# Kernel optimization log

Measured on AMD Instinct MI355X. Metric: run time of the kernel, lower is better.

## Reference

```python
import jax, jax.numpy as jnp
import numpy as np

B, T, D_MODEL, D_FF, NUM_EXPERTS, TOP_K = 8, 4096, 512, 2048, 8, 2
VOCAB = 50257


def setup_inputs() -> dict:
    key = jax.random.key(0)
    k_x, k_id, k_w1, k_w2 = jax.random.split(key, 4)
    x = jax.random.normal(k_x, (B, T, D_MODEL), dtype=jnp.float32)
    token_ids = jax.random.randint(k_id, (B, T), 0, VOCAB, dtype=jnp.int32)
    # stacked expert MLP params: Linear(D,F) -> GELU -> Linear(F,D)
    W1 = jax.random.normal(k_w1, (NUM_EXPERTS, D_MODEL, D_FF), dtype=jnp.float32) * 0.02
    b1 = jnp.zeros((NUM_EXPERTS, D_FF), dtype=jnp.float32)
    W2 = jax.random.normal(k_w2, (NUM_EXPERTS, D_FF, D_MODEL), dtype=jnp.float32) * 0.02
    b2 = jnp.zeros((NUM_EXPERTS, D_MODEL), dtype=jnp.float32)
    return {"x": x, "token_ids": token_ids, "W1": W1, "b1": b1, "W2": W2, "b2": b2}


def reference(x, token_ids, W1, b1, W2, b2):
    Bx, Tx, D = x.shape
    E = W1.shape[0]
    top_k = TOP_K
    # hash routing: expert_ids[b,t,k] = (b*T + token_ids[b,t] + k) % E
    rows = (jnp.arange(Bx, dtype=jnp.int32) * Tx)[:, None, None]           # (B,1,1)
    offs = jnp.arange(top_k, dtype=jnp.int32)                               # (K,)
    expert_ids = (rows + token_ids[:, :, None] + offs) % E                  # (B,T,K)
    onehot = jax.nn.one_hot(expert_ids, E, dtype=jnp.float32)               # (B,T,K,E)
    hits = onehot.sum(axis=2)                                               # (B,T,E) hit counts
    # per-hit combine weight in torch source: (1/top_k)/top_k = 1/top_k^2
    comb_w = hits / float(top_k * top_k)
    # masked-dense expert MLP == dense MLP on x with output masked (per-token ops)
    out = jnp.zeros_like(x)
    for e in range(E):  # fixed small loop over experts
        h = jax.nn.gelu(x @ W1[e] + b1[e], approximate=False)               # (B,T,F)
        y = h @ W2[e] + b2[e]                                               # (B,T,D)
        out = out + y * comb_w[..., e:e + 1]
    expert_counts = hits.sum(axis=(0, 1))                                   # (E,)
    return out, expert_ids, expert_counts
```

## Files before the change

kernel.cpp:

```cpp
#include <hip/hip_runtime.h>
#include <math.h>

#define NUM_E 8
#define NTOK  32768
#define TSEQ  4096
#define DM    512
#define DF    2048
#define CAP   6144

typedef unsigned short ushort_t;
typedef __attribute__((ext_vector_type(8))) short short8;
typedef __attribute__((ext_vector_type(4))) float floatx4;

__device__ __forceinline__ unsigned short f2bf(float f){
  union { float f; unsigned int u; } v; v.f = f;
  unsigned int u = v.u;
  unsigned int r = (u + 0x7FFFu + ((u >> 16) & 1u)) >> 16;
  return (unsigned short)r;
}

__device__ __forceinline__ float gelu_fast(float h){
  float z = h * (1.5957691216057308f + 0.0713548162726009f * h * h);
  float e = __expf(-z);
  return h * __builtin_amdgcn_rcpf(1.0f + e);
}

__device__ __forceinline__ void gld_lds16(const void* g, void* l){
  __builtin_amdgcn_global_load_lds(
      (const __attribute__((address_space(1))) unsigned int*)g,
      (__attribute__((address_space(3))) unsigned int*)l, 16, 0, 0);
}

__global__ void k_init(int* cnt){
  if (threadIdx.x < NUM_E) cnt[threadIdx.x] = 0;
}

__global__ __launch_bounds__(1024) void k_route(
    const int* __restrict__ tok, float* __restrict__ ids_out,
    int* __restrict__ cnt, int* __restrict__ list){
  __shared__ int lcnt[NUM_E];
  __shared__ int lbase[NUM_E];
  int tid = threadIdx.x;
  if (tid < NUM_E) lcnt[tid] = 0;
  __syncthreads();
  int flat = blockIdx.x * 1024 + tid;
  int b = flat >> 12;
  int t = tok[flat];
  int base = b * TSEQ + t;
  int e0 = base & 7;
  int e1 = (base + 1) & 7;
  ids_out[2*flat]   = (float)e0;
  ids_out[2*flat+1] = (float)e1;
  int lpos = atomicAdd(&lcnt[e0], 1);
  __syncthreads();
  if (tid < NUM_E) lbase[tid] = atomicAdd(&cnt[tid], lcnt[tid]);
  __syncthreads();
  int pos = lbase[e0] + lpos;
  if (pos < CAP) list[e0*CAP + pos] = flat;
}

__global__ void k_finalize(const int* __restrict__ cnt, int* __restrict__ off,
                           float* __restrict__ counts_out){
  int tid = threadIdx.x;
  if (tid == 0){
    int s = 0;
    for (int c = 0; c < NUM_E; c++){ off[c] = s; s += cnt[c]; }
    off[NUM_E] = s;
  }
  if (tid < NUM_E)
    counts_out[tid] = (float)(cnt[tid] + cnt[(tid + 7) & 7]);
}

__global__ __launch_bounds__(256) void k_prep(
    const float* __restrict__ x, ushort_t* __restrict__ xb,
    const float* __restrict__ W1, ushort_t* __restrict__ w1t,
    const float* __restrict__ W2, ushort_t* __restrict__ w2t){
  int b = blockIdx.x;
  if (b < 16384){
    int i = b*256 + threadIdx.x;
    float4 v = ((const float4*)x)[i];
    ushort4 o;
    o.x = f2bf(v.x); o.y = f2bf(v.y); o.z = f2bf(v.z); o.w = f2bf(v.w);
    ((ushort4*)xb)[i] = o;
    return;
  }
  __shared__ ushort_t s[64][65];
  const float* in; ushort_t* out; int R, C, c0, r0, perm;
  if (b < 18432){
    int t = b - 16384; int e = t >> 8; int rem = t & 255;
    R = DM; C = DF;
    in  = W1 + (size_t)e * R * C;
    out = w1t + (size_t)e * R * C;
    c0 = (rem & 31) * 64; r0 = (rem >> 5) * 64; perm = 0;
  } else {
    int t = b - 18432; int e = t >> 8; int rem = t & 255;
    R = DF; C = DM;
    in  = W2 + (size_t)e * R * C;
    out = w2t + (size_t)e * R * C;
    c0 = (rem & 7) * 64; r0 = (rem >> 3) * 64; perm = 1;
  }
  int tx = threadIdx.x & 63, ty = threadIdx.x >> 6;
  for (int rr = ty; rr < 64; rr += 4)
    s[rr][tx] = f2bf(in[(size_t)(r0+rr)*C + c0 + tx]);
  __syncthreads();
  int sx = perm ? ((tx & 3)*16 + (tx >> 2)) : tx;
  for (int cc = ty; cc < 64; cc += 4)
    out[(size_t)(c0+cc)*R + r0 + tx] = s[sx][cc];
}


__global__ __launch_bounds__(256, 4) void k_gemm1(
    const ushort_t* __restrict__ xb, const ushort_t* __restrict__ w1t,
    const float* __restrict__ b1,
    const int* __restrict__ cnt, const int* __restrict__ off,
    const int* __restrict__ list, ushort_t* __restrict__ H, int c0)
{
  int c = c0 + (blockIdx.z >> 1), slot = blockIdx.z & 1;
  int e = (c + slot) & 7;
  int n_c = cnt[c];
  int m0 = blockIdx.x * 128;
  if (m0 >= n_c) return;
  int n0 = blockIdx.y * 128;

  __shared__ alignas(16) ushort_t As[128*64];
  __shared__ alignas(16) ushort_t Bs[128*64];
  __shared__ unsigned int rowoff[128];

  int tid = threadIdx.x;
  int lane = tid & 63, w = tid >> 6;

  if (tid < 128){
    int i = m0 + tid;
    int tk = list[c*CAP + ((i < n_c) ? i : 0)];
    rowoff[tid] = (unsigned int)tk * (DM*2);
  }
  __syncthreads();

  int rl = lane >> 3;
  int cc = (lane & 7) ^ rl;
  unsigned int aoff[4], boff[4];
  const char* w1te = (const char*)w1t + (size_t)e * ((size_t)DF*DM*2);
  #pragma unroll
  for (int j = 0; j < 4; j++){
    int r = j*32 + w*8 + rl;
    aoff[j] = rowoff[r] + (unsigned int)cc*16u;
    boff[j] = (unsigned int)(n0 + r) * (DM*2) + (unsigned int)cc*16u;
  }

  floatx4 acc[4][4];
  #pragma unroll
  for (int a = 0; a < 4; a++)
    #pragma unroll
    for (int q = 0; q < 4; q++) acc[a][q] = floatx4{0.f,0.f,0.f,0.f};

  int wr = w >> 1, wc = w & 1;
  int col = lane & 15, quad = lane >> 4;
  int xa = col & 7;
  const ushort_t* A0 = As + (wr*64 + col)*64 + (quad ^ xa)*8;
  const ushort_t* A1 = As + (wr*64 + col)*64 + ((quad + 4) ^ xa)*8;
  const ushort_t* B0 = Bs + (wc*64 + col)*64 + (quad ^ xa)*8;
  const ushort_t* B1 = Bs + (wc*64 + col)*64 + ((quad + 4) ^ xa)*8;
  char* AsW = (char*)As + w*1024;
  char* BsW = (char*)Bs + w*1024;

  for (int k0 = 0; k0 < DM; k0 += 64){
    #pragma unroll
    for (int j = 0; j < 4; j++){
      gld_lds16((const char*)xb + aoff[j] + k0*2, AsW + j*4096);
      gld_lds16(w1te + boff[j] + k0*2, BsW + j*4096);
    }
    __syncthreads();
    {
      short8 a[4], bfr[4];
      #pragma unroll
      for (int mi = 0; mi < 4; mi++) a[mi] = *(const short8*)(A0 + mi*1024);
      #pragma unroll
      for (int ni = 0; ni < 4; ni++) bfr[ni] = *(const short8*)(B0 + ni*1024);
      #pragma unroll
      for (int mi = 0; mi < 4; mi++)
        #pragma unroll
        for (int ni = 0; ni < 4; ni++)
          acc[mi][ni] = __builtin_amdgcn_mfma_f32_16x16x32_bf16(a[mi], bfr[ni], acc[mi][ni], 0, 0, 0);
      #pragma unroll
      for (int mi = 0; mi < 4; mi++) a[mi] = *(const short8*)(A1 + mi*1024);
      #pragma unroll
      for (int ni = 0; ni < 4; ni++) bfr[ni] = *(const short8*)(B1 + ni*1024);
      #pragma unroll
      for (int mi = 0; mi < 4; mi++)
        #pragma unroll
        for (int ni = 0; ni < 4; ni++)
          acc[mi][ni] = __builtin_amdgcn_mfma_f32_16x16x32_bf16(a[mi], bfr[ni], acc[mi][ni], 0, 0, 0);
    }
    __syncthreads();
  }

  int hbase = off[c] - off[c0];
  const float* b1p = b1 + e*DF + n0 + wc*64;
  float bias[4];
  #pragma unroll
  for (int ni = 0; ni < 4; ni++) bias[ni] = b1p[ni*16 + col];
  ushort_t* hcol = H + (size_t)slot*DF + n0 + wc*64 + col*4;
  #pragma unroll
  for (int mi = 0; mi < 4; mi++){
    #pragma unroll
    for (int r = 0; r < 4; r++){
      int m = wr*64 + mi*16 + quad*4 + r;
      int i = m0 + m;
      if (i < n_c){
        ushort4 o;
        o.x = f2bf(gelu_fast(acc[mi][0][r] + bias[0]));
        o.y = f2bf(gelu_fast(acc[mi][1][r] + bias[1]));
        o.z = f2bf(gelu_fast(acc[mi][2][r] + bias[2]));
        o.w = f2bf(gelu_fast(acc[mi][3][r] + bias[3]));
        *(ushort4*)(hcol + (size_t)(hbase + i)*(2*DF)) = o;
      }
    }
  }
}

__global__ __launch_bounds__(256, 4) void k_gemm2(
    const ushort_t* __restrict__ H, const ushort_t* __restrict__ w2t,
    const float* __restrict__ b2,
    const int* __restrict__ cnt, const int* __restrict__ off,
    const int* __restrict__ list, float* __restrict__ out, int c0, int nb)
{
  int c = c0 + blockIdx.z;
  int e1 = (c + 1) & 7;
  int n_c = cnt[c];
  int m0 = blockIdx.x * 128;
  if (m0 >= n_c) return;
  int n0 = blockIdx.y * 128;

  __shared__ alignas(16) ushort_t As[128*64];
  __shared__ alignas(16) ushort_t Bs[128*64];
  __shared__ int rowtok[128];

  int tid = threadIdx.x;
  int lane = tid & 63, w = tid >> 6;
  int rowbase = off[c] - off[c0];
  int phaseTok = off[c0 + nb] - off[c0];

  if (tid < 128){
    int i = m0 + tid;
    rowtok[tid] = list[c*CAP + ((i < n_c) ? i : 0)];
  }

  int rl = lane >> 3;
  int cc = (lane & 7) ^ rl;
  unsigned int aoff[4], boff[4];
  #pragma unroll
  for (int j = 0; j < 4; j++){
    int r = j*32 + w*8 + rl;
    int rg = rowbase + m0 + r;
    if (rg > phaseTok - 1) rg = phaseTok - 1;
    aoff[j] = (unsigned int)rg * (2*DF*2) + (unsigned int)cc*16u;
    boff[j] = (unsigned int)(n0 + r) * (DF*2) + (unsigned int)cc*16u;
  }
  const char* bb0 = (const char*)w2t + (size_t)c  * ((size_t)DM*DF*2);
  const char* bb1 = (const char*)w2t + (size_t)e1 * ((size_t)DM*DF*2);

  floatx4 acc[4][4];
  #pragma unroll
  for (int a = 0; a < 4; a++)
    #pragma unroll
    for (int q = 0; q < 4; q++) acc[a][q] = floatx4{0.f,0.f,0.f,0.f};

  int wr = w >> 1, wc = w & 1;
  int col = lane & 15, quad = lane >> 4;
  int xa = col & 7;
  const ushort_t* A0 = As + (wr*64 + col)*64 + (quad ^ xa)*8;
  const ushort_t* A1 = As + (wr*64 + col)*64 + ((quad + 4) ^ xa)*8;
  const ushort_t* B0 = Bs + (wc*64 + col)*64 + (quad ^ xa)*8;
  const ushort_t* B1 = Bs + (wc*64 + col)*64 + ((quad + 4) ^ xa)*8;
  char* AsW = (char*)As + w*1024;
  char* BsW = (char*)Bs + w*1024;

  for (int k0 = 0; k0 < 2*DF; k0 += 64){
    const char* bb = (k0 < DF) ? (bb0 + k0*2) : (bb1 + (k0 - DF)*2);
    #pragma unroll
    for (int j = 0; j < 4; j++){
      gld_lds16((const char*)H + aoff[j] + k0*2, AsW + j*4096);
      gld_lds16(bb + boff[j], BsW + j*4096);
    }
    __syncthreads();
    {
      short8 a[4], bfr[4];
      #pragma unroll
      for (int mi = 0; mi < 4; mi++) a[mi] = *(const short8*)(A0 + mi*1024);
      #pragma unroll
      for (int ni = 0; ni < 4; ni++) bfr[ni] = *(const short8*)(B0 + ni*1024);
      #pragma unroll
      for (int mi = 0; mi < 4; mi++)
        #pragma unroll
        for (int ni = 0; ni < 4; ni++)
          acc[mi][ni] = __builtin_amdgcn_mfma_f32_16x16x32_bf16(a[mi], bfr[ni], acc[mi][ni], 0, 0, 0);
      #pragma unroll
      for (int mi = 0; mi < 4; mi++) a[mi] = *(const short8*)(A1 + mi*1024);
      #pragma unroll
      for (int ni = 0; ni < 4; ni++) bfr[ni] = *(const short8*)(B1 + ni*1024);
      #pragma unroll
      for (int mi = 0; mi < 4; mi++)
        #pragma unroll
        for (int ni = 0; ni < 4; ni++)
          acc[mi][ni] = __builtin_amdgcn_mfma_f32_16x16x32_bf16(a[mi], bfr[ni], acc[mi][ni], 0, 0, 0);
    }
    __syncthreads();
  }

  const float* b2a = b2 + c*DM;
  const float* b2b = b2 + e1*DM;
  #pragma unroll
  for (int mi = 0; mi < 4; mi++){
    #pragma unroll
    for (int r = 0; r < 4; r++){
      int m = wr*64 + mi*16 + quad*4 + r;
      int i = m0 + m;
      if (i < n_c){
        int tk = rowtok[m];
        float* orow = out + (size_t)tk*DM + n0 + wc*64;
        #pragma unroll
        for (int ni = 0; ni < 4; ni++){
          int nl = ni*16 + col;
          int gn = n0 + wc*64 + nl;
          orow[nl] = 0.25f * (acc[mi][ni][r] + b2a[gn] + b2b[gn]);
        }
      }
    }
  }
}

extern "C" void kernel_launch(void* const* d_in, const int* in_sizes, int n_in,
                              void* d_out, int out_size, void* d_ws, size_t ws_size,
                              hipStream_t stream){
  const float* x   = (const float*)d_in[0];
  const int*   tok = (const int*)d_in[1];
  const float* W1  = (const float*)d_in[2];
  const float* b1  = (const float*)d_in[3];
  const float* W2  = (const float*)d_in[4];
  const float* b2  = (const float*)d_in[5];

  float* out        = (float*)d_out;
  float* ids_out    = out + (size_t)NTOK*DM;
  float* counts_out = ids_out + (size_t)NTOK*2;

  char* ws = (char*)d_ws;
  int* cnt  = (int*)ws;
  int* off  = cnt + 16;
  int* list = (int*)(ws + 4096);
  ushort_t* w1t = (ushort_t*)(ws + (1 << 20));
  ushort_t* w2t = w1t + (size_t)NUM_E*DF*DM;
  ushort_t* xb  = w2t + (size_t)NUM_E*DM*DF;
  ushort_t* H   = (ushort_t*)(ws + (65ull << 20));

  size_t fixed_b = 65ull << 20;
  size_t avail = (ws_size > fixed_b) ? (ws_size - fixed_b) : 0;
  int nb = 0;
  for (int cand = 8; cand >= 1; cand >>= 1){
    size_t need = ((size_t)cand * 4096 + 1024) * (size_t)(2*DF) * 2;
    if (need <= avail){ nb = cand; break; }
  }
  if (nb == 0) nb = 1;

  k_init<<<1, 64, 0, stream>>>(cnt);
  k_route<<<NTOK/1024, 1024, 0, stream>>>(tok, ids_out, cnt, list);
  k_finalize<<<1, 64, 0, stream>>>(cnt, off, counts_out);
  k_prep<<<20480, 256, 0, stream>>>(x, xb, W1, w1t, W2, w2t);

  for (int c0 = 0; c0 < NUM_E; c0 += nb){
    k_gemm1<<<dim3(CAP/128, DF/128, 2*nb), 256, 0, stream>>>(
        xb, w1t, b1, cnt, off, list, H, c0);
    k_gemm2<<<dim3(CAP/128, DM/128, nb), 256, 0, stream>>>(
        H, w2t, b2, cnt, off, list, out, c0, nb);
  }
}
```

Before: 525.2 us.

## Software-pipeline expert GEMM phases with double-buffered H and merge setup kernels

Merges the init, route and prep kernels into one setup kernel, using a memset and 1024-thread blocks. Splits the experts into phases of two and double-buffers the H intermediate, so one fused launch runs the GEMM2 of the previous phase alongside the GEMM1 of the current one. This is meant to fill the GPU better and cut the tail and idle gaps between dependent launches. The cost is a larger workspace need, grid blocks with mismatched y extent that exit early, and a phase size fixed at two that drops the earlier adaptive batching.

```diff
diff --git a/kernel.cpp b/kernel.cpp
--- a/kernel.cpp
+++ b/kernel.cpp
@@ -7,6 +7,7 @@
 #define DM    512
 #define DF    2048
 #define CAP   6144
+#define PHROWS 8704
 
 typedef unsigned short ushort_t;
 typedef __attribute__((ext_vector_type(8))) short short8;
@@ -31,32 +32,70 @@
       (__attribute__((address_space(3))) unsigned int*)l, 16, 0, 0);
 }
 
-__global__ void k_init(int* cnt){
-  if (threadIdx.x < NUM_E) cnt[threadIdx.x] = 0;
-}
-
-__global__ __launch_bounds__(1024) void k_route(
+__global__ __launch_bounds__(1024) void k_setup(
     const int* __restrict__ tok, float* __restrict__ ids_out,
-    int* __restrict__ cnt, int* __restrict__ list){
+    int* __restrict__ cnt, int* __restrict__ list,
+    const float* __restrict__ x, ushort_t* __restrict__ xb,
+    const float* __restrict__ W1, ushort_t* __restrict__ w1t,
+    const float* __restrict__ W2, ushort_t* __restrict__ w2t)
+{
   __shared__ int lcnt[NUM_E];
   __shared__ int lbase[NUM_E];
+  __shared__ ushort_t s[4][64][65];
+  int b = blockIdx.x;
   int tid = threadIdx.x;
-  if (tid < NUM_E) lcnt[tid] = 0;
+
+  if (b < 32){
+    if (tid < NUM_E) lcnt[tid] = 0;
+    __syncthreads();
+    int flat = b * 1024 + tid;
+    int bb = flat >> 12;
+    int t = tok[flat];
+    int base = bb * TSEQ + t;
+    int e0 = base & 7;
+    int e1 = (base + 1) & 7;
+    ids_out[2*flat]   = (float)e0;
+    ids_out[2*flat+1] = (float)e1;
+    int lpos = atomicAdd(&lcnt[e0], 1);
+    __syncthreads();
+    if (tid < NUM_E) lbase[tid] = atomicAdd(&cnt[tid], lcnt[tid]);
+    __syncthreads();
+    int pos = lbase[e0] + lpos;
+    if (pos < CAP) list[e0*CAP + pos] = flat;
+    return;
+  }
+  if (b < 32 + 4096){
+    int i = (b - 32)*1024 + tid;
+    float4 v = ((const float4*)x)[i];
+    ushort4 o;
+    o.x = f2bf(v.x); o.y = f2bf(v.y); o.z = f2bf(v.z); o.w = f2bf(v.w);
+    ((ushort4*)xb)[i] = o;
+    return;
+  }
+  int sub = tid >> 8, t8 = tid & 255;
+  int tx = t8 & 63, ty = t8 >> 6;
+  const float* in; ushort_t* out; int R, C, c0t, r0, perm;
+  if (b < 32 + 4096 + 512){
+    int tile = (b - (32 + 4096))*4 + sub;
+    int e = tile >> 8, rem = tile & 255;
+    R = DM; C = DF;
+    in  = W1 + (size_t)e * R * C;
+    out = w1t + (size_t)e * R * C;
+    c0t = (rem & 31) * 64; r0 = (rem >> 5) * 64; perm = 0;
+  } else {
+    int tile = (b - (32 + 4096 + 512))*4 + sub;
+    int e = tile >> 8, rem = tile & 255;
+    R = DF; C = DM;
+    in  = W2 + (size_t)e * R * C;
+    out = w2t + (size_t)e * R * C;
+    c0t = (rem & 7) * 64; r0 = (rem >> 3) * 64; perm = 1;
+  }
+  for (int rr = ty; rr < 64; rr += 4)
+    s[sub][rr][tx] = f2bf(in[(size_t)(r0+rr)*C + c0t + tx]);
   __syncthreads();
-  int flat = blockIdx.x * 1024 + tid;
-  int b = flat >> 12;
-  int t = tok[flat];
-  int base = b * TSEQ + t;
-  int e0 = base & 7;
-  int e1 = (base + 1) & 7;
-  ids_out[2*flat]   = (float)e0;
-  ids_out[2*flat+1] = (float)e1;
-  int lpos = atomicAdd(&lcnt[e0], 1);
-  __syncthreads();
-  if (tid < NUM_E) lbase[tid] = atomicAdd(&cnt[tid], lcnt[tid]);
-  __syncthreads();
-  int pos = lbase[e0] + lpos;
-  if (pos < CAP) list[e0*CAP + pos] = flat;
+  int sx = perm ? ((tx & 3)*16 + (tx >> 2)) : tx;
+  for (int ccx = ty; ccx < 64; ccx += 4)
+    out[(size_t)(c0t+ccx)*R + r0 + tx] = s[sub][sx][ccx];
 }
 
 __global__ void k_finalize(const int* __restrict__ cnt, int* __restrict__ off,
@@ -71,60 +110,23 @@
     counts_out[tid] = (float)(cnt[tid] + cnt[(tid + 7) & 7]);
 }
 
-__global__ __launch_bounds__(256) void k_prep(
-    const float* __restrict__ x, ushort_t* __restrict__ xb,
-    const float* __restrict__ W1, ushort_t* __restrict__ w1t,
-    const float* __restrict__ W2, ushort_t* __restrict__ w2t){
-  int b = blockIdx.x;
-  if (b < 16384){
-    int i = b*256 + threadIdx.x;
-    float4 v = ((const float4*)x)[i];
-    ushort4 o;
-    o.x = f2bf(v.x); o.y = f2bf(v.y); o.z = f2bf(v.z); o.w = f2bf(v.w);
-    ((ushort4*)xb)[i] = o;
-    return;
-  }
-  __shared__ ushort_t s[64][65];
-  const float* in; ushort_t* out; int R, C, c0, r0, perm;
-  if (b < 18432){
-    int t = b - 16384; int e = t >> 8; int rem = t & 255;
-    R = DM; C = DF;
-    in  = W1 + (size_t)e * R * C;
-    out = w1t + (size_t)e * R * C;
-    c0 = (rem & 31) * 64; r0 = (rem >> 5) * 64; perm = 0;
-  } else {
-    int t = b - 18432; int e = t >> 8; int rem = t & 255;
-    R = DF; C = DM;
-    in  = W2 + (size_t)e * R * C;
-    out = w2t + (size_t)e * R * C;
-    c0 = (rem & 7) * 64; r0 = (rem >> 3) * 64; perm = 1;
-  }
-  int tx = threadIdx.x & 63, ty = threadIdx.x >> 6;
-  for (int rr = ty; rr < 64; rr += 4)
-    s[rr][tx] = f2bf(in[(size_t)(r0+rr)*C + c0 + tx]);
-  __syncthreads();
-  int sx = perm ? ((tx & 3)*16 + (tx >> 2)) : tx;
-  for (int cc = ty; cc < 64; cc += 4)
-    out[(size_t)(c0+cc)*R + r0 + tx] = s[sx][cc];
-}
-
-
-__global__ __launch_bounds__(256, 4) void k_gemm1(
-    const ushort_t* __restrict__ xb, const ushort_t* __restrict__ w1t,
-    const float* __restrict__ b1,
-    const int* __restrict__ cnt, const int* __restrict__ off,
-    const int* __restrict__ list, ushort_t* __restrict__ H, int c0)
+
+__device__ __forceinline__ void gemm1_body(
+    char* smem, const ushort_t* __restrict__ xb, const ushort_t* __restrict__ w1t,
+    const float* __restrict__ b1, const int* __restrict__ cnt,
+    const int* __restrict__ off, const int* __restrict__ list,
+    ushort_t* __restrict__ H, int c0, int zz)
 {
-  int c = c0 + (blockIdx.z >> 1), slot = blockIdx.z & 1;
+  ushort_t* As = (ushort_t*)smem;
+  ushort_t* Bs = (ushort_t*)(smem + 16384);
+  unsigned int* rowoff = (unsigned int*)(smem + 32768);
+
+  int c = c0 + (zz >> 1), slot = zz & 1;
   int e = (c + slot) & 7;
   int n_c = cnt[c];
   int m0 = blockIdx.x * 128;
   if (m0 >= n_c) return;
   int n0 = blockIdx.y * 128;
-
-  __shared__ alignas(16) ushort_t As[128*64];
-  __shared__ alignas(16) ushort_t Bs[128*64];
-  __shared__ unsigned int rowoff[128];
 
   int tid = threadIdx.x;
   int lane = tid & 63, w = tid >> 6;
@@ -218,27 +220,27 @@
   }
 }
 
-__global__ __launch_bounds__(256, 4) void k_gemm2(
-    const ushort_t* __restrict__ H, const ushort_t* __restrict__ w2t,
-    const float* __restrict__ b2,
-    const int* __restrict__ cnt, const int* __restrict__ off,
-    const int* __restrict__ list, float* __restrict__ out, int c0, int nb)
+__device__ __forceinline__ void gemm2_body(
+    char* smem, const ushort_t* __restrict__ H, const ushort_t* __restrict__ w2t,
+    const float* __restrict__ b2, const int* __restrict__ cnt,
+    const int* __restrict__ off, const int* __restrict__ list,
+    float* __restrict__ out, int c0, int zz)
 {
-  int c = c0 + blockIdx.z;
+  ushort_t* As = (ushort_t*)smem;
+  ushort_t* Bs = (ushort_t*)(smem + 16384);
+  int* rowtok = (int*)(smem + 32768);
+
+  int c = c0 + zz;
   int e1 = (c + 1) & 7;
   int n_c = cnt[c];
   int m0 = blockIdx.x * 128;
   if (m0 >= n_c) return;
   int n0 = blockIdx.y * 128;
 
-  __shared__ alignas(16) ushort_t As[128*64];
-  __shared__ alignas(16) ushort_t Bs[128*64];
-  __shared__ int rowtok[128];
-
   int tid = threadIdx.x;
   int lane = tid & 63, w = tid >> 6;
   int rowbase = off[c] - off[c0];
-  int phaseTok = off[c0 + nb] - off[c0];
+  int phaseTok = off[c0 + 2] - off[c0];
 
   if (tid < 128){
     int i = m0 + tid;
@@ -329,6 +331,27 @@
   }
 }
 
+__global__ __launch_bounds__(256, 4) void k_fused(
+    const ushort_t* __restrict__ xb, const ushort_t* __restrict__ w1t,
+    const float* __restrict__ b1,
+    const ushort_t* __restrict__ w2t, const float* __restrict__ b2,
+    const int* __restrict__ cnt, const int* __restrict__ off,
+    const int* __restrict__ list,
+    ushort_t* __restrict__ H0, ushort_t* __restrict__ H1,
+    float* __restrict__ out, int p, int g2z)
+{
+  __shared__ char smem[33280];
+  int zz = blockIdx.z;
+  if (zz < g2z){
+    if (blockIdx.y >= DM/128) return;
+    const ushort_t* Hr = ((p - 1) & 1) ? H1 : H0;
+    gemm2_body(smem, Hr, w2t, b2, cnt, off, list, out, 2*(p-1), zz);
+  } else {
+    ushort_t* Hw = (p & 1) ? H1 : H0;
+    gemm1_body(smem, xb, w1t, b1, cnt, off, list, Hw, 2*p, zz - g2z);
+  }
+}
+
 extern "C" void kernel_launch(void* const* d_in, const int* in_sizes, int n_in,
                               void* d_out, int out_size, void* d_ws, size_t ws_size,
                               hipStream_t stream){
@@ -350,26 +373,32 @@
   ushort_t* w1t = (ushort_t*)(ws + (1 << 20));
   ushort_t* w2t = w1t + (size_t)NUM_E*DF*DM;
   ushort_t* xb  = w2t + (size_t)NUM_E*DM*DF;
-  ushort_t* H   = (ushort_t*)(ws + (65ull << 20));
+  ushort_t* H0  = (ushort_t*)(ws + (65ull << 20));
 
   size_t fixed_b = 65ull << 20;
   size_t avail = (ws_size > fixed_b) ? (ws_size - fixed_b) : 0;
-  int nb = 0;
-  for (int cand = 8; cand >= 1; cand >>= 1){
-    size_t need = ((size_t)cand * 4096 + 1024) * (size_t)(2*DF) * 2;
-    if (need <= avail){ nb = cand; break; }
-  }
-  if (nb == 0) nb = 1;
-
-  k_init<<<1, 64, 0, stream>>>(cnt);
-  k_route<<<NTOK/1024, 1024, 0, stream>>>(tok, ids_out, cnt, list);
+  size_t phbytes = (size_t)PHROWS * (2*DF) * sizeof(ushort_t);
+  int overlap = (avail >= 2*phbytes) ? 1 : 0;
+  ushort_t* H1 = overlap ? (H0 + (size_t)PHROWS * (2*DF)) : H0;
+
+  hipMemsetAsync(cnt, 0, 64, stream);
+  k_setup<<<32 + 4096 + 512 + 512, 1024, 0, stream>>>(
+      tok, ids_out, cnt, list, x, xb, W1, w1t, W2, w2t);
   k_finalize<<<1, 64, 0, stream>>>(cnt, off, counts_out);
-  k_prep<<<20480, 256, 0, stream>>>(x, xb, W1, w1t, W2, w2t);
-
-  for (int c0 = 0; c0 < NUM_E; c0 += nb){
-    k_gemm1<<<dim3(CAP/128, DF/128, 2*nb), 256, 0, stream>>>(
-        xb, w1t, b1, cnt, off, list, H, c0);
-    k_gemm2<<<dim3(CAP/128, DM/128, nb), 256, 0, stream>>>(
-        H, w2t, b2, cnt, off, list, out, c0, nb);
-  }
-}
+
+  if (overlap){
+    for (int p = 0; p <= 4; p++){
+      int g2z = (p > 0) ? 2 : 0;
+      int g1z = (p < 4) ? 4 : 0;
+      k_fused<<<dim3(CAP/128, DF/128, g2z + g1z), 256, 0, stream>>>(
+          xb, w1t, b1, w2t, b2, cnt, off, list, H0, H1, out, p, g2z);
+    }
+  } else {
+    for (int p = 0; p < 4; p++){
+      k_fused<<<dim3(CAP/128, DF/128, 4), 256, 0, stream>>>(
+          xb, w1t, b1, w2t, b2, cnt, off, list, H0, H1, out, p, 0);
+      k_fused<<<dim3(CAP/128, DM/128, 2), 256, 0, stream>>>(
+          xb, w1t, b1, w2t, b2, cnt, off, list, H0, H1, out, p + 1, 2);
+    }
+  }
+}
```

Result: slower. 565.0 us (+7.6%).
